# Kernel optimization log

Hardware: AMD Instinct MI355X
Metric: run time of the kernel (lower is better)

The kernel has to match this reference:

```python
import jax, jax.numpy as jnp
import numpy as np

REACH = 3
NEG_SLOPE = 0.01
NBINS = 256


def _conv(x, w, b=None):
    y = jax.lax.conv_general_dilated(x, w, (1, 1), 'VALID',
                                     dimension_numbers=('NCHW', 'OIHW', 'NCHW'))
    if b is not None:
        y = y + b[None, :, None, None]
    return y


def _causal_conv(x, wT, bT, wL, w1, b1, w2, b2, w3, b3):
    # top context: drop last row, pad (left=3,right=3,top=3), kernel (3,7) -> [N,32,H,W]
    xt = _conv(jnp.pad(x[:, :, :-1, :], ((0, 0), (0, 0), (REACH, 0), (REACH, REACH))), wT, bT)
    # left context: drop last col, pad left=3, kernel (1,3) -> [N,32,H,W]
    xl = _conv(jnp.pad(x[:, :, :, :-1], ((0, 0), (0, 0), (0, 0), (REACH, 0))), wL)
    h = jax.nn.leaky_relu(xt + xl, NEG_SLOPE)
    h = jax.nn.leaky_relu(_conv(h, w1, b1), NEG_SLOPE)
    h = jax.nn.leaky_relu(_conv(h, w2, b2), NEG_SLOPE)
    return jnp.clip(_conv(h, w3, b3), -1.0, 1.0)


def _pred_median3(x, a, b, c):
    med = jnp.maximum(jnp.minimum(a, jnp.maximum(b, c)), jnp.minimum(b, c))
    return jnp.fmod(x - med + 1.0, 2.0) - 1.0


def _calc_rmse(x):
    return 255.0 * jnp.sqrt(jnp.mean(jnp.square(x)))


def _calc_invCR(x):
    # x: [N,1,H,W]; per-channel 256-bin histogram over [-1,1], entropy in bits
    n = x.shape[0]
    res = x.shape[2] * x.shape[3]
    xf = x.reshape(n, res)
    idx = jnp.clip(jnp.floor((xf + 1.0) * (NBINS / 2.0)), 0, NBINS - 1).astype(jnp.int32)
    mask = ((xf >= -1.0) & (xf <= 1.0)).astype(xf.dtype)  # histc ignores out-of-range
    hist = jax.vmap(lambda i, m: jnp.zeros((NBINS,), xf.dtype).at[i].add(m))(idx, mask)
    p = hist / res
    ent = jnp.sum(jnp.where(p > 0, -p * jnp.log2(jnp.where(p > 0, p, 1.0)), 0.0))
    return ent / (8.0 * n)


def setup_inputs() -> dict:
    key = jax.random.key(0)
    ks = jax.random.split(key, 32)
    d = {}
    d['x'] = jax.random.uniform(ks[0], (4, 3, 512, 512), jnp.float32, -1.0, 1.0)
    i = 1
    for p in ['a', 'b', 'c']:
        d[p + '_wT'] = jax.random.normal(ks[i], (32, 1, 3, 7), jnp.float32) / np.float32(np.sqrt(21.0)); i += 1
        d[p + '_bT'] = jax.random.normal(ks[i], (32,), jnp.float32) * np.float32(0.01); i += 1
        d[p + '_wL'] = jax.random.normal(ks[i], (32, 1, 1, 3), jnp.float32) / np.float32(np.sqrt(3.0)); i += 1
        d[p + '_w1'] = jax.random.normal(ks[i], (32, 32, 1, 1), jnp.float32) / np.float32(np.sqrt(32.0)); i += 1
        d[p + '_b1'] = jax.random.normal(ks[i], (32,), jnp.float32) * np.float32(0.01); i += 1
        d[p + '_w2'] = jax.random.normal(ks[i], (32, 32, 1, 1), jnp.float32) / np.float32(np.sqrt(32.0)); i += 1
        d[p + '_b2'] = jax.random.normal(ks[i], (32,), jnp.float32) * np.float32(0.01); i += 1
        d[p + '_w3'] = jax.random.normal(ks[i], (1, 32, 1, 1), jnp.float32) / np.float32(np.sqrt(32.0)); i += 1
        d[p + '_b3'] = jax.random.normal(ks[i], (1,), jnp.float32) * np.float32(0.01); i += 1
    return d


def reference(x, a_wT, a_bT, a_wL, a_w1, a_b1, a_w2, a_b2, a_w3, a_b3,
              b_wT, b_bT, b_wL, b_w1, b_b1, b_w2, b_b2, b_w3, b_b3,
              c_wT, c_bT, c_wL, c_w1, c_b1, c_w2, c_b2, c_w3, c_b3):
    b, c, h, w = x.shape
    xr = x.reshape(b * c, 1, h, w)
    pa = _causal_conv(xr, a_wT, a_bT, a_wL, a_w1, a_b1, a_w2, a_b2, a_w3, a_b3)
    pb = _causal_conv(xr, b_wT, b_bT, b_wL, b_w1, b_b1, b_w2, b_b2, b_w3, b_b3)
    pc = _causal_conv(xr, c_wT, c_bT, c_wL, c_w1, c_b1, c_w2, c_b2, c_w3, c_b3)
    deltas = _pred_median3(xr, pa, pb, pc)
    loss1 = _calc_rmse(deltas)
    loss0 = _calc_rmse(xr)
    invCR0 = _calc_invCR(xr)
    invCR1 = _calc_invCR(deltas)
    return loss1, loss0, invCR0, invCR1
```

## Files before the change

### kernel.cpp

```cpp
#include <hip/hip_runtime.h>
#include <hip/hip_bf16.h>
#include <cmath>

#define HH 512
#define WW 512
#define NIMG 12
#define RES (HH*WW)
#define NBINS 256
#define PXB 512

typedef __attribute__((ext_vector_type(8))) short bf8;
typedef __attribute__((ext_vector_type(4))) float f32x4;

__device__ __forceinline__ unsigned bf_rne(float x) {
    unsigned u = __float_as_uint(x);
    return (u + 0x7fffu + ((u >> 16) & 1u)) >> 16;
}
__device__ __forceinline__ float lk(float a) { return fmaxf(a, 0.01f * a); }

__device__ __forceinline__ unsigned cvtpk(float a, float b) {
    unsigned r;
    asm("v_cvt_pk_bf16_f32 %0, %1, %2" : "=v"(r) : "v"(a), "v"(b));
    return r;
}

union bf8u { bf8 f; unsigned u[4]; };

__device__ __forceinline__ bf8 actfrag(const f32x4 a0, const f32x4 a1) {
    bf8u r;
    r.u[0] = cvtpk(lk(a0[0]), lk(a0[1]));
    r.u[1] = cvtpk(lk(a0[2]), lk(a0[3]));
    r.u[2] = cvtpk(lk(a1[0]), lk(a1[1]));
    r.u[3] = cvtpk(lk(a1[2]), lk(a1[3]));
    return r.f;
}

__device__ __forceinline__ bf8 slow_build(const float* __restrict__ X,
                                          int i, int jb, int m16, int q)
{
    const int jc = jb + m16;
    bf8 pf;
    #pragma unroll
    for (int j = 0; j < 8; ++j) {
        const int k = 8*q + j;
        float v = 0.0f;
        if (k < 21) {
            const int rr = i - 3 + k/7;
            const int cc = jc - 3 + k%7;
            if (rr >= 0 && cc >= 0 && cc < WW) v = X[rr*WW + cc];
        } else if (k < 24) {
            const int cc = jc - 3 + (k - 21);
            if (cc >= 0) v = X[i*WW + cc];
        } else if (k == 24) {
            v = 1.0f;
        }
        pf[j] = (short)bf_rne(v);
    }
    return pf;
}

#define MFMA(A, B, C) __builtin_amdgcn_mfma_f32_16x16x32_bf16((A), (B), (C), 0, 0, 0)

__device__ __forceinline__ void run_pred_tile(
    const bf8 w0a, const bf8 w0b,
    const bf8 w1a, const bf8 w1b,
    const bf8 w2a, const bf8 w2b,
    const bf8 w3f,
    const f32x4 c10, const f32x4 c11, const f32x4 c20, const f32x4 c21,
    const bf8 pf, f32x4& acc3)
{
    const f32x4 z = {0.f, 0.f, 0.f, 0.f};
    f32x4 za = MFMA(w0a, pf, z);
    f32x4 zb = MFMA(w0b, pf, z);
    bf8 h = actfrag(za, zb);
    za = MFMA(w1a, h, c10);
    zb = MFMA(w1b, h, c11);
    h = actfrag(za, zb);
    za = MFMA(w2a, h, c20);
    zb = MFMA(w2b, h, c21);
    h = actfrag(za, zb);
    acc3 = MFMA(w3f, h, acc3);
}

__global__ __launch_bounds__(192, 4) void codec_main(
    const float* __restrict__ x,
    const float* __restrict__ a_wT, const float* __restrict__ a_bT, const float* __restrict__ a_wL,
    const float* __restrict__ a_w1, const float* __restrict__ a_b1,
    const float* __restrict__ a_w2, const float* __restrict__ a_b2,
    const float* __restrict__ a_w3, const float* __restrict__ a_b3,
    const float* __restrict__ b_wT, const float* __restrict__ b_bT, const float* __restrict__ b_wL,
    const float* __restrict__ b_w1, const float* __restrict__ b_b1,
    const float* __restrict__ b_w2, const float* __restrict__ b_b2,
    const float* __restrict__ b_w3, const float* __restrict__ b_b3,
    const float* __restrict__ c_wT, const float* __restrict__ c_bT, const float* __restrict__ c_wL,
    const float* __restrict__ c_w1, const float* __restrict__ c_b1,
    const float* __restrict__ c_w2, const float* __restrict__ c_b2,
    const float* __restrict__ c_w3, const float* __restrict__ c_b3,
    float* __restrict__ sums,
    unsigned* __restrict__ hist_x,
    unsigned* __restrict__ hist_d)
{
    __shared__ float predb[3][PXB];
    __shared__ unsigned shx[NBINS], shd[NBINS];
    __shared__ float red[8];

    const int tid  = threadIdx.x;
    const int lane = tid & 63;
    const int wv   = tid >> 6;
    const int q    = lane >> 4;
    const int m16  = lane & 15;

    for (int k = tid; k < NBINS; k += 192) { shx[k] = 0u; shd[k] = 0u; }

    const float* wT = (wv == 0) ? a_wT : ((wv == 1) ? b_wT : c_wT);
    const float* bT = (wv == 0) ? a_bT : ((wv == 1) ? b_bT : c_bT);
    const float* wL = (wv == 0) ? a_wL : ((wv == 1) ? b_wL : c_wL);
    const float* w1 = (wv == 0) ? a_w1 : ((wv == 1) ? b_w1 : c_w1);
    const float* b1 = (wv == 0) ? a_b1 : ((wv == 1) ? b_b1 : c_b1);
    const float* w2 = (wv == 0) ? a_w2 : ((wv == 1) ? b_w2 : c_w2);
    const float* b2 = (wv == 0) ? a_b2 : ((wv == 1) ? b_b2 : c_b2);
    const float* w3 = (wv == 0) ? a_w3 : ((wv == 1) ? b_w3 : c_w3);
    const float* b3 = (wv == 0) ? a_b3 : ((wv == 1) ? b_b3 : c_b3);

    bf8 wA0[2], wA1[2], wA2[2], aw3;
    f32x4 cb1[2], cb2[2];
    #pragma unroll
    for (int mt = 0; mt < 2; ++mt) {
        const int ch = ((m16 >> 2) << 3) + (mt << 2) + (m16 & 3);
        bf8 f0;
        #pragma unroll
        for (int j = 0; j < 8; ++j) {
            const int k = 8*q + j;
            float v = 0.0f;
            if (k < 21)       v = wT[ch*21 + k];
            else if (k < 24)  v = wL[ch*3 + (k - 21)];
            else if (k == 24) v = bT[ch];
            f0[j] = (short)bf_rne(v);
        }
        wA0[mt] = f0;
        {
            const f32x4 lo = *(const f32x4*)&w1[ch*32 + 8*q];
            const f32x4 hi = *(const f32x4*)&w1[ch*32 + 8*q + 4];
            bf8 g;
            #pragma unroll
            for (int j = 0; j < 4; ++j) { g[j] = (short)bf_rne(lo[j]); g[4+j] = (short)bf_rne(hi[j]); }
            wA1[mt] = g;
        }
        {
            const f32x4 lo = *(const f32x4*)&w2[ch*32 + 8*q];
            const f32x4 hi = *(const f32x4*)&w2[ch*32 + 8*q + 4];
            bf8 g;
            #pragma unroll
            for (int j = 0; j < 4; ++j) { g[j] = (short)bf_rne(lo[j]); g[4+j] = (short)bf_rne(hi[j]); }
            wA2[mt] = g;
        }
        if (mt == 0) { cb1[0] = *(const f32x4*)&b1[8*q];     cb2[0] = *(const f32x4*)&b2[8*q]; }
        else         { cb1[1] = *(const f32x4*)&b1[8*q + 4]; cb2[1] = *(const f32x4*)&b2[8*q + 4]; }
    }
    {
        bf8 g;
        #pragma unroll
        for (int j = 0; j < 8; ++j) {
            const float v = (m16 == 0) ? w3[8*q + j] : 0.0f;
            g[j] = (short)bf_rne(v);
        }
        aw3 = g;
    }
    f32x4 bias3v = {0.f, 0.f, 0.f, 0.f};
    if (q == 0) bias3v[0] = b3[0];

    const int img = blockIdx.y;
    const float* __restrict__ X = x + (size_t)img * RES;
    const char*  Xc = (const char*)X;
    const int bx = blockIdx.x;
    const int i  = ((bx & 7) << 6) | (bx >> 3);

    int koff[8];
    #pragma unroll
    for (int j = 0; j < 8; ++j) {
        const int k = 8*q + j;
        int row, col;
        if (k < 21)      { row = i - 3 + k/7; col = m16 - 3 + k%7; }
        else if (k < 24) { row = i;           col = m16 - 3 + (k - 21); }
        else             { row = i;           col = m16; }
        koff[j] = (row*WW + col) * 4;
    }
    const bool rowsafe = (i >= 3);

    #pragma unroll 1
    for (int u = 0; u < 8; ++u) {
        bf8 pf0, pf1, pf2, pf3;
        #pragma unroll
        for (int t = 0; t < 4; ++t) {
            const int tt = 4*u + t;
            const bool fast = rowsafe && (tt >= 1) && (tt <= 30);
            bf8 pf;
            if (fast) {
                float nf[8];
                #pragma unroll
                for (int j = 0; j < 8; ++j)
                    nf[j] = *(const float*)(Xc + koff[j] + 64*t);
                bf8u r;
                if (q < 3) {
                    r.u[0] = cvtpk(nf[0], nf[1]); r.u[1] = cvtpk(nf[2], nf[3]);
                    r.u[2] = cvtpk(nf[4], nf[5]); r.u[3] = cvtpk(nf[6], nf[7]);
                } else {
                    r.u[0] = 0x00003f80u; r.u[1] = 0u; r.u[2] = 0u; r.u[3] = 0u;
                }
                pf = r.f;
            } else {
                pf = slow_build(X, i, 16*tt, m16, q);
            }
            if (t == 0) pf0 = pf; else if (t == 1) pf1 = pf;
            else if (t == 2) pf2 = pf; else pf3 = pf;
        }

        f32x4 acc0 = bias3v, acc1 = bias3v, acc2 = bias3v, acc3 = bias3v;
        run_pred_tile(wA0[0], wA0[1], wA1[0], wA1[1], wA2[0], wA2[1], aw3,
                      cb1[0], cb1[1], cb2[0], cb2[1], pf0, acc0);
        run_pred_tile(wA0[0], wA0[1], wA1[0], wA1[1], wA2[0], wA2[1], aw3,
                      cb1[0], cb1[1], cb2[0], cb2[1], pf1, acc1);
        run_pred_tile(wA0[0], wA0[1], wA1[0], wA1[1], wA2[0], wA2[1], aw3,
                      cb1[0], cb1[1], cb2[0], cb2[1], pf2, acc2);
        run_pred_tile(wA0[0], wA0[1], wA1[0], wA1[1], wA2[0], wA2[1], aw3,
                      cb1[0], cb1[1], cb2[0], cb2[1], pf3, acc3);

        if (q == 0) {
            predb[wv][64*u      + m16] = fminf(fmaxf(acc0[0], -1.0f), 1.0f);
            predb[wv][64*u + 16 + m16] = fminf(fmaxf(acc1[0], -1.0f), 1.0f);
            predb[wv][64*u + 32 + m16] = fminf(fmaxf(acc2[0], -1.0f), 1.0f);
            predb[wv][64*u + 48 + m16] = fminf(fmaxf(acc3[0], -1.0f), 1.0f);
        }

        #pragma unroll
        for (int j = 0; j < 8; ++j) koff[j] += 256;
    }

    __syncthreads();

    float sx = 0.0f, sd = 0.0f;
    const float* __restrict__ Xrow = X + i*WW;
    for (int idx = tid; idx < PXB; idx += 192) {
        const float xv = Xrow[idx];
        const float pa = predb[0][idx];
        const float pb = predb[1][idx];
        const float pc = predb[2][idx];
        const float med = fmaxf(fminf(pa, fmaxf(pb, pc)), fminf(pb, pc));
        const float delta = fmodf(xv - med + 1.0f, 2.0f) - 1.0f;
        int bx2 = (int)floorf((xv + 1.0f) * 128.0f);
        bx2 = bx2 < 0 ? 0 : (bx2 > 255 ? 255 : bx2);
        if (xv >= -1.0f && xv <= 1.0f) atomicAdd(&shx[bx2], 1u);
        int bd = (int)floorf((delta + 1.0f) * 128.0f);
        bd = bd < 0 ? 0 : (bd > 255 ? 255 : bd);
        if (delta >= -1.0f && delta <= 1.0f) atomicAdd(&shd[bd], 1u);
        sx += xv*xv; sd += delta*delta;
    }

    #pragma unroll
    for (int off = 32; off > 0; off >>= 1) {
        sx += __shfl_down(sx, off);
        sd += __shfl_down(sd, off);
    }
    if (lane == 0) { red[wv] = sx; red[4 + wv] = sd; }
    __syncthreads();
    if (tid == 0) {
        atomicAdd(&sums[0], red[0] + red[1] + red[2]);
        atomicAdd(&sums[1], red[4] + red[5] + red[6]);
    }
    for (int k = tid; k < NBINS; k += 192) {
        if (shx[k]) atomicAdd(&hist_x[img*NBINS + k], shx[k]);
        if (shd[k]) atomicAdd(&hist_d[img*NBINS + k], shd[k]);
    }
}

__global__ __launch_bounds__(256) void codec_final(
    const float* __restrict__ sums,
    const unsigned* __restrict__ hist_x,
    const unsigned* __restrict__ hist_d,
    float* __restrict__ out)
{
    __shared__ float red[16];
    const int tid = threadIdx.x;
    float ex = 0.0f, ed = 0.0f;
    const float inv_res = 1.0f / (float)RES;
    for (int k = tid; k < NIMG*NBINS; k += 256) {
        const unsigned hx = hist_x[k];
        const unsigned hd = hist_d[k];
        if (hx) { const float p = (float)hx * inv_res; ex -= p * log2f(p); }
        if (hd) { const float p = (float)hd * inv_res; ed -= p * log2f(p); }
    }
    #pragma unroll
    for (int off = 32; off > 0; off >>= 1) {
        ex += __shfl_down(ex, off);
        ed += __shfl_down(ed, off);
    }
    const int lane = tid & 63, wv = tid >> 6;
    if (lane == 0) { red[wv] = ex; red[8 + wv] = ed; }
    __syncthreads();
    if (tid == 0) {
        const float Ex = red[0] + red[1] + red[2] + red[3];
        const float Ed = red[8] + red[9] + red[10] + red[11];
        const float inv_n = 1.0f / (float)(NIMG * RES);
        out[0] = 255.0f * sqrtf(sums[1] * inv_n);
        out[1] = 255.0f * sqrtf(sums[0] * inv_n);
        out[2] = Ex / (8.0f * (float)NIMG);
        out[3] = Ed / (8.0f * (float)NIMG);
    }
}

extern "C" void kernel_launch(void* const* d_in, const int* in_sizes, int n_in,
                              void* d_out, int out_size, void* d_ws, size_t ws_size,
                              hipStream_t stream)
{
    const float* x = (const float*)d_in[0];
    const float* w[27];
    for (int k = 0; k < 27; ++k) w[k] = (const float*)d_in[1 + k];

    float*    sums   = (float*)d_ws;
    unsigned* hist_x = (unsigned*)((char*)d_ws + 16);
    unsigned* hist_d = hist_x + NIMG*NBINS;
    const size_t zbytes = 16 + (size_t)2*NIMG*NBINS*sizeof(unsigned);
    hipMemsetAsync(d_ws, 0, zbytes, stream);

    dim3 grid(HH, NIMG);
    codec_main<<<grid, dim3(192), 0, stream>>>(
        x,
        w[0],  w[1],  w[2],  w[3],  w[4],  w[5],  w[6],  w[7],  w[8],
        w[9],  w[10], w[11], w[12], w[13], w[14], w[15], w[16], w[17],
        w[18], w[19], w[20], w[21], w[22], w[23], w[24], w[25], w[26],
        sums, hist_x, hist_d);
    codec_final<<<1, dim3(256), 0, stream>>>(sums, hist_x, hist_d, (float*)d_out);
}
```

Measured before the change: 311.3 us.

## Stage packed bf16 input rows in LDS and pack leaky-relu multiplies

Each block now cooperatively loads the four needed input rows once, converts them to packed bf16 pairs in two column-parity copies, and stores them in shared memory. The per-tile patch fragments are then read as four dwords from LDS, which removes the scattered per-lane global gathers and the branchy slow path at borders. Other changes: leaky-relu uses v_pk_mul_f32 on pairs, the first-layer weight layout is rearranged to match the new fragment packing, tiles are processed two at a time, and launch bounds rise to 5 blocks per CU. Costs are an extra barrier plus LDS usage and possible register pressure from the higher occupancy target.

After: 320.5 us. 3.0% more time.

```diff
diff --git a/kernel.cpp b/kernel.cpp
--- a/kernel.cpp
+++ b/kernel.cpp
@@ -11,52 +11,39 @@
 
 typedef __attribute__((ext_vector_type(8))) short bf8;
 typedef __attribute__((ext_vector_type(4))) float f32x4;
+typedef __attribute__((ext_vector_type(2))) float f32x2;
 
 __device__ __forceinline__ unsigned bf_rne(float x) {
     unsigned u = __float_as_uint(x);
     return (u + 0x7fffu + ((u >> 16) & 1u)) >> 16;
 }
-__device__ __forceinline__ float lk(float a) { return fmaxf(a, 0.01f * a); }
 
 __device__ __forceinline__ unsigned cvtpk(float a, float b) {
     unsigned r;
     asm("v_cvt_pk_bf16_f32 %0, %1, %2" : "=v"(r) : "v"(a), "v"(b));
     return r;
 }
+__device__ __forceinline__ f32x2 pkmul(f32x2 a, f32x2 b) {
+    f32x2 r;
+    asm("v_pk_mul_f32 %0, %1, %2" : "=v"(r) : "v"(a), "v"(b));
+    return r;
+}
 
 union bf8u { bf8 f; unsigned u[4]; };
 
-__device__ __forceinline__ bf8 actfrag(const f32x4 a0, const f32x4 a1) {
+__device__ __forceinline__ unsigned actpair(float x0, float x1, f32x2 k) {
+    f32x2 a; a[0] = x0; a[1] = x1;
+    const f32x2 p = pkmul(a, k);
+    return cvtpk(fmaxf(x0, p[0]), fmaxf(x1, p[1]));
+}
+
+__device__ __forceinline__ bf8 actfrag(const f32x4 a0, const f32x4 a1, f32x2 k) {
     bf8u r;
-    r.u[0] = cvtpk(lk(a0[0]), lk(a0[1]));
-    r.u[1] = cvtpk(lk(a0[2]), lk(a0[3]));
-    r.u[2] = cvtpk(lk(a1[0]), lk(a1[1]));
-    r.u[3] = cvtpk(lk(a1[2]), lk(a1[3]));
+    r.u[0] = actpair(a0[0], a0[1], k);
+    r.u[1] = actpair(a0[2], a0[3], k);
+    r.u[2] = actpair(a1[0], a1[1], k);
+    r.u[3] = actpair(a1[2], a1[3], k);
     return r.f;
-}
-
-__device__ __forceinline__ bf8 slow_build(const float* __restrict__ X,
-                                          int i, int jb, int m16, int q)
-{
-    const int jc = jb + m16;
-    bf8 pf;
-    #pragma unroll
-    for (int j = 0; j < 8; ++j) {
-        const int k = 8*q + j;
-        float v = 0.0f;
-        if (k < 21) {
-            const int rr = i - 3 + k/7;
-            const int cc = jc - 3 + k%7;
-            if (rr >= 0 && cc >= 0 && cc < WW) v = X[rr*WW + cc];
-        } else if (k < 24) {
-            const int cc = jc - 3 + (k - 21);
-            if (cc >= 0) v = X[i*WW + cc];
-        } else if (k == 24) {
-            v = 1.0f;
-        }
-        pf[j] = (short)bf_rne(v);
-    }
-    return pf;
 }
 
 #define MFMA(A, B, C) __builtin_amdgcn_mfma_f32_16x16x32_bf16((A), (B), (C), 0, 0, 0)
@@ -67,22 +54,33 @@
     const bf8 w2a, const bf8 w2b,
     const bf8 w3f,
     const f32x4 c10, const f32x4 c11, const f32x4 c20, const f32x4 c21,
-    const bf8 pf, f32x4& acc3)
+    const bf8 pf, f32x4& acc3, const f32x2 k)
 {
     const f32x4 z = {0.f, 0.f, 0.f, 0.f};
     f32x4 za = MFMA(w0a, pf, z);
     f32x4 zb = MFMA(w0b, pf, z);
-    bf8 h = actfrag(za, zb);
+    bf8 h = actfrag(za, zb, k);
     za = MFMA(w1a, h, c10);
     zb = MFMA(w1b, h, c11);
-    h = actfrag(za, zb);
+    h = actfrag(za, zb, k);
     za = MFMA(w2a, h, c20);
     zb = MFMA(w2b, h, c21);
-    h = actfrag(za, zb);
+    h = actfrag(za, zb, k);
     acc3 = MFMA(w3f, h, acc3);
 }
 
-__global__ __launch_bounds__(192, 4) void codec_main(
+__device__ __forceinline__ bf8 build_pf(const unsigned* __restrict__ rb, int tt, int q) {
+    bf8u r;
+    r.u[0] = rb[8*tt + 0];
+    r.u[1] = rb[8*tt + 1];
+    unsigned u2 = rb[8*tt + 2];
+    unsigned u3 = rb[8*tt + 3];
+    if (q == 3) { u2 = 0x00003f80u; u3 = 0u; }
+    r.u[2] = u2; r.u[3] = u3;
+    return r.f;
+}
+
+__global__ __launch_bounds__(192, 5) void codec_main(
     const float* __restrict__ x,
     const float* __restrict__ a_wT, const float* __restrict__ a_bT, const float* __restrict__ a_wL,
     const float* __restrict__ a_w1, const float* __restrict__ a_b1,
@@ -100,6 +98,7 @@
     unsigned* __restrict__ hist_x,
     unsigned* __restrict__ hist_d)
 {
+    __shared__ unsigned rowbuf[4][2][260];
     __shared__ float predb[3][PXB];
     __shared__ unsigned shx[NBINS], shd[NBINS];
     __shared__ float red[8];
@@ -130,11 +129,9 @@
         bf8 f0;
         #pragma unroll
         for (int j = 0; j < 8; ++j) {
-            const int k = 8*q + j;
             float v = 0.0f;
-            if (k < 21)       v = wT[ch*21 + k];
-            else if (k < 24)  v = wL[ch*3 + (k - 21)];
-            else if (k == 24) v = bT[ch];
+            if (q < 3) { if (j < 7) v = wT[ch*21 + q*7 + j]; }
+            else       { if (j < 3) v = wL[ch*3 + j]; else if (j == 4) v = bT[ch]; }
             f0[j] = (short)bf_rne(v);
         }
         wA0[mt] = f0;
@@ -169,71 +166,61 @@
     f32x4 bias3v = {0.f, 0.f, 0.f, 0.f};
     if (q == 0) bias3v[0] = b3[0];
 
+    f32x2 k001; k001[0] = 0.01f; k001[1] = 0.01f;
+
     const int img = blockIdx.y;
     const float* __restrict__ X = x + (size_t)img * RES;
-    const char*  Xc = (const char*)X;
     const int bx = blockIdx.x;
     const int i  = ((bx & 7) << 6) | (bx >> 3);
 
-    int koff[8];
-    #pragma unroll
-    for (int j = 0; j < 8; ++j) {
-        const int k = 8*q + j;
-        int row, col;
-        if (k < 21)      { row = i - 3 + k/7; col = m16 - 3 + k%7; }
-        else if (k < 24) { row = i;           col = m16 - 3 + (k - 21); }
-        else             { row = i;           col = m16; }
-        koff[j] = (row*WW + col) * 4;
-    }
-    const bool rowsafe = (i >= 3);
+    for (int w = tid; w < 4*520; w += 192) {
+        const int r   = w / 520;
+        const int rem = w - r*520;
+        const int cp  = rem / 260;
+        const int wd  = rem - cp*260;
+        const int srcrow = (r < 3) ? (i - 3 + r) : i;
+        const int p0 = 2*wd - 4 + cp;
+        float f0 = 0.0f, f1 = 0.0f;
+        if (srcrow >= 0) {
+            if ((unsigned)p0 < (unsigned)WW)       f0 = X[srcrow*WW + p0];
+            if ((unsigned)(p0+1) < (unsigned)WW)   f1 = X[srcrow*WW + p0 + 1];
+        }
+        rowbuf[r][cp][wd] = cvtpk(f0, f1);
+    }
+    __syncthreads();
+
+    const int cp = 1 - (m16 & 1);
+    const int w0 = (m16 + 1) >> 1;
+    const unsigned* __restrict__ rb = &rowbuf[q][cp][w0];
 
     #pragma unroll 1
     for (int u = 0; u < 8; ++u) {
-        bf8 pf0, pf1, pf2, pf3;
-        #pragma unroll
-        for (int t = 0; t < 4; ++t) {
-            const int tt = 4*u + t;
-            const bool fast = rowsafe && (tt >= 1) && (tt <= 30);
-            bf8 pf;
-            if (fast) {
-                float nf[8];
-                #pragma unroll
-                for (int j = 0; j < 8; ++j)
-                    nf[j] = *(const float*)(Xc + koff[j] + 64*t);
-                bf8u r;
-                if (q < 3) {
-                    r.u[0] = cvtpk(nf[0], nf[1]); r.u[1] = cvtpk(nf[2], nf[3]);
-                    r.u[2] = cvtpk(nf[4], nf[5]); r.u[3] = cvtpk(nf[6], nf[7]);
-                } else {
-                    r.u[0] = 0x00003f80u; r.u[1] = 0u; r.u[2] = 0u; r.u[3] = 0u;
-                }
-                pf = r.f;
-            } else {
-                pf = slow_build(X, i, 16*tt, m16, q);
+        {
+            const bf8 pfa = build_pf(rb, 4*u + 0, q);
+            const bf8 pfb = build_pf(rb, 4*u + 1, q);
+            f32x4 acc0 = bias3v, acc1 = bias3v;
+            run_pred_tile(wA0[0], wA0[1], wA1[0], wA1[1], wA2[0], wA2[1], aw3,
+                          cb1[0], cb1[1], cb2[0], cb2[1], pfa, acc0, k001);
+            run_pred_tile(wA0[0], wA0[1], wA1[0], wA1[1], wA2[0], wA2[1], aw3,
+                          cb1[0], cb1[1], cb2[0], cb2[1], pfb, acc1, k001);
+            if (q == 0) {
+                predb[wv][64*u      + m16] = fminf(fmaxf(acc0[0], -1.0f), 1.0f);
+                predb[wv][64*u + 16 + m16] = fminf(fmaxf(acc1[0], -1.0f), 1.0f);
             }
-            if (t == 0) pf0 = pf; else if (t == 1) pf1 = pf;
-            else if (t == 2) pf2 = pf; else pf3 = pf;
-        }
-
-        f32x4 acc0 = bias3v, acc1 = bias3v, acc2 = bias3v, acc3 = bias3v;
-        run_pred_tile(wA0[0], wA0[1], wA1[0], wA1[1], wA2[0], wA2[1], aw3,
-                      cb1[0], cb1[1], cb2[0], cb2[1], pf0, acc0);
-        run_pred_tile(wA0[0], wA0[1], wA1[0], wA1[1], wA2[0], wA2[1], aw3,
-                      cb1[0], cb1[1], cb2[0], cb2[1], pf1, acc1);
-        run_pred_tile(wA0[0], wA0[1], wA1[0], wA1[1], wA2[0], wA2[1], aw3,
-                      cb1[0], cb1[1], cb2[0], cb2[1], pf2, acc2);
-        run_pred_tile(wA0[0], wA0[1], wA1[0], wA1[1], wA2[0], wA2[1], aw3,
-                      cb1[0], cb1[1], cb2[0], cb2[1], pf3, acc3);
-
-        if (q == 0) {
-            predb[wv][64*u      + m16] = fminf(fmaxf(acc0[0], -1.0f), 1.0f);
-            predb[wv][64*u + 16 + m16] = fminf(fmaxf(acc1[0], -1.0f), 1.0f);
-            predb[wv][64*u + 32 + m16] = fminf(fmaxf(acc2[0], -1.0f), 1.0f);
-            predb[wv][64*u + 48 + m16] = fminf(fmaxf(acc3[0], -1.0f), 1.0f);
-        }
-
-        #pragma unroll
-        for (int j = 0; j < 8; ++j) koff[j] += 256;
+        }
+        {
+            const bf8 pfa = build_pf(rb, 4*u + 2, q);
+            const bf8 pfb = build_pf(rb, 4*u + 3, q);
+            f32x4 acc0 = bias3v, acc1 = bias3v;
+            run_pred_tile(wA0[0], wA0[1], wA1[0], wA1[1], wA2[0], wA2[1], aw3,
+                          cb1[0], cb1[1], cb2[0], cb2[1], pfa, acc0, k001);
+            run_pred_tile(wA0[0], wA0[1], wA1[0], wA1[1], wA2[0], wA2[1], aw3,
+                          cb1[0], cb1[1], cb2[0], cb2[1], pfb, acc1, k001);
+            if (q == 0) {
+                predb[wv][64*u + 32 + m16] = fminf(fmaxf(acc0[0], -1.0f), 1.0f);
+                predb[wv][64*u + 48 + m16] = fminf(fmaxf(acc1[0], -1.0f), 1.0f);
+            }
+        }
     }
 
     __syncthreads();
```
